# Kernel optimization log

Measured on AMD Instinct MI355X. Metric: run time of the kernel, lower is better.

## Reference

```python
import jax, jax.numpy as jnp
import numpy as np

B, C, H, W, D = 2, 256, 16, 16, 16
CQK = C // 8  # 32


def setup_inputs() -> dict:
    key = jax.random.key(0)
    ks = jax.random.split(key, 6)
    x = jax.random.normal(ks[0], (B, C, H, W, D), dtype=jnp.float32)
    wq = jax.random.normal(ks[1], (CQK, C), dtype=jnp.float32) * (1.0 / np.sqrt(C))
    wk = jax.random.normal(ks[2], (CQK, C), dtype=jnp.float32) * (1.0 / np.sqrt(C))
    wv = jax.random.normal(ks[3], (C, C), dtype=jnp.float32) * (1.0 / np.sqrt(C))
    bq = jnp.zeros((CQK,), dtype=jnp.float32)
    bk = jnp.zeros((CQK,), dtype=jnp.float32)
    bv = jnp.zeros((C,), dtype=jnp.float32)
    gamma_pam = jax.random.normal(ks[4], (1,), dtype=jnp.float32)
    gamma_cam = jax.random.normal(ks[5], (1,), dtype=jnp.float32)
    return {"x": x, "wq": wq, "bq": bq, "wk": wk, "bk": bk,
            "wv": wv, "bv": bv, "gamma_pam": gamma_pam, "gamma_cam": gamma_cam}


def _da_block(x, wq, bq, wk, bk, wv, bv, gamma_pam, gamma_cam):
    b, c, h, w, d = x.shape
    n = h * w * d
    xf = x.reshape(b, c, n)  # (B, C, N)

    # ---- PAM (position attention) ----
    # 1x1x1 Conv3d == per-voxel channel matmul
    q = jnp.einsum('oc,bcn->bon', wq, xf) + bq[None, :, None]  # (B, CQK, N)
    k = jnp.einsum('oc,bcn->bon', wk, xf) + bk[None, :, None]  # (B, CQK, N)
    v = jnp.einsum('oc,bcn->bon', wv, xf) + bv[None, :, None]  # (B, C, N)
    energy = jnp.einsum('bci,bcj->bij', q, k)                  # (B, N, N)
    attn = jax.nn.softmax(energy, axis=-1)
    # out[b,c,i] = sum_j v[b,c,j] * attn[b,i,j]
    pam_out = jnp.einsum('bcj,bij->bci', v, attn)              # (B, C, N)
    x1 = gamma_pam[0] * pam_out.reshape(b, c, h, w, d) + x

    # ---- CAM (channel attention, max-inverted energy) ----
    energy_c = jnp.einsum('bin,bjn->bij', xf, xf)              # (B, C, C)
    energy_new = jnp.max(energy_c, axis=-1, keepdims=True) - energy_c
    attn_c = jax.nn.softmax(energy_new, axis=-1)
    cam_out = jnp.einsum('bij,bjn->bin', attn_c, xf)           # (B, C, N)
    x2 = gamma_cam[0] * cam_out.reshape(b, c, h, w, d) + x

    return x1 + x2


def reference(x, wq, bq, wk, bk, wv, bv, gamma_pam, gamma_cam):
    return _da_block(x, wq, bq, wk, bk, wv, bv, gamma_pam, gamma_cam)
```

## Files before the change

### kernel.cpp

```cpp
#include <hip/hip_runtime.h>
#include <hip/hip_bf16.h>


#define B_ 2
#define C_ 256
#define N_ 4096
#define QK_ 32

#define TJ_ 128
#define PPB_ 136

typedef __hip_bfloat16 bf16;
typedef __attribute__((ext_vector_type(8))) short bf16x8f;
typedef __attribute__((ext_vector_type(4))) float f32x4;

union bf8pack { bf16 h[8]; int4 v; bf16x8f f; };
union bf4pack { bf16 h[4]; uint2 u; };

__global__ __launch_bounds__(256) void k_wcv(
    const float* __restrict__ wq, const float* __restrict__ wk, const float* __restrict__ wv,
    bf16* __restrict__ wqkh, bf16* __restrict__ wqkl,
    bf16* __restrict__ wvh, bf16* __restrict__ wvl) {
  int idx = blockIdx.x * 256 + threadIdx.x;
  if (idx < 64 * C_) {
    int r = idx >> 8, c = idx & 255;
    float v = (r < 32) ? wq[r * C_ + c] : wk[(r - 32) * C_ + c];
    bf16 h = __float2bfloat16(v);
    wqkh[idx] = h; wqkl[idx] = __float2bfloat16(v - __bfloat162float(h));
  } else {
    int j = idx - 64 * C_;
    float v = wv[j];
    bf16 h = __float2bfloat16(v);
    wvh[j] = h; wvl[j] = __float2bfloat16(v - __bfloat162float(h));
  }
}

__global__ __launch_bounds__(256) void k_xt(
    const float* __restrict__ x, bf16* __restrict__ xthi, bf16* __restrict__ xtlo,
    bf16* __restrict__ xchi, bf16* __restrict__ xclo) {
  int b = blockIdx.z;
  int c0 = blockIdx.y * 64;
  int n0 = blockIdx.x * 64;
  __shared__ float t[64 * 65];
  int tid = threadIdx.x;
  int col = tid & 63, rowq = tid >> 6;
#pragma unroll
  for (int k = 0; k < 16; k++) {
    int r = k * 4 + rowq;
    size_t src = ((size_t)b * C_ + c0 + r) * N_ + n0 + col;
    float v = x[src];
    t[r * 65 + col] = v;
    bf16 h = __float2bfloat16(v);
    xchi[src] = h;
    xclo[src] = __float2bfloat16(v - __bfloat162float(h));
  }
  __syncthreads();
#pragma unroll
  for (int k = 0; k < 16; k++) {
    int nrow = k * 4 + rowq;
    float v = t[col * 65 + nrow];
    bf16 h = __float2bfloat16(v);
    size_t o = ((size_t)b * N_ + n0 + nrow) * C_ + c0 + col;
    xthi[o] = h;
    xtlo[o] = __float2bfloat16(v - __bfloat162float(h));
  }
}

__global__ __launch_bounds__(256) void k_qkp(
    const bf16* __restrict__ xthi, const bf16* __restrict__ xtlo,
    const bf16* __restrict__ wqkh, const bf16* __restrict__ wqkl,
    const float* __restrict__ bq, const float* __restrict__ bk,
    bf16* __restrict__ qhi, bf16* __restrict__ qlo,
    bf16* __restrict__ khi, bf16* __restrict__ klo) {
  int b = blockIdx.y;
  int tid = threadIdx.x;
  int lane = tid & 63, wave = tid >> 6;
  int n16 = lane & 15, quad = lane >> 4;
  int nb = blockIdx.x * 128 + wave * 32;

  f32x4 acc[4][2];
#pragma unroll
  for (int ot = 0; ot < 4; ot++)
#pragma unroll
    for (int nt = 0; nt < 2; nt++) acc[ot][nt] = (f32x4)(0.f);

#pragma unroll
  for (int kk = 0; kk < 8; kk++) {
    bf16x8f Ah[4], Al[4], Bh[2], Bl[2];
#pragma unroll
    for (int ot = 0; ot < 4; ot++) {
      size_t off = (size_t)(ot * 16 + n16) * C_ + kk * 32 + quad * 8;
      Ah[ot] = *(const bf16x8f*)(const void*)(wqkh + off);
      Al[ot] = *(const bf16x8f*)(const void*)(wqkl + off);
    }
#pragma unroll
    for (int nt = 0; nt < 2; nt++) {
      size_t off = ((size_t)b * N_ + nb + nt * 16 + n16) * C_ + kk * 32 + quad * 8;
      Bh[nt] = *(const bf16x8f*)(const void*)(xthi + off);
      Bl[nt] = *(const bf16x8f*)(const void*)(xtlo + off);
    }
#pragma unroll
    for (int ot = 0; ot < 4; ot++)
#pragma unroll
      for (int nt = 0; nt < 2; nt++) {
        acc[ot][nt] = __builtin_amdgcn_mfma_f32_16x16x32_bf16(Ah[ot], Bh[nt], acc[ot][nt], 0, 0, 0);
        acc[ot][nt] = __builtin_amdgcn_mfma_f32_16x16x32_bf16(Al[ot], Bh[nt], acc[ot][nt], 0, 0, 0);
        acc[ot][nt] = __builtin_amdgcn_mfma_f32_16x16x32_bf16(Ah[ot], Bl[nt], acc[ot][nt], 0, 0, 0);
      }
  }
#pragma unroll
  for (int ot = 0; ot < 4; ot++)
#pragma unroll
    for (int nt = 0; nt < 2; nt++) {
      int n = nb + nt * 16 + n16;
      int o0 = (ot & 1) * 16 + quad * 4;
      bf4pack ph, pl;
#pragma unroll
      for (int r = 0; r < 4; r++) {
        float v = acc[ot][nt][r] + (ot < 2 ? bq[o0 + r] : bk[o0 + r]);
        bf16 h = __float2bfloat16(v);
        ph.h[r] = h; pl.h[r] = __float2bfloat16(v - __bfloat162float(h));
      }
      size_t base = ((size_t)b * N_ + n) * QK_ + o0;
      if (ot < 2) { *(uint2*)(qhi + base) = ph.u; *(uint2*)(qlo + base) = pl.u; }
      else        { *(uint2*)(khi + base) = ph.u; *(uint2*)(klo + base) = pl.u; }
    }
}

__global__ __launch_bounds__(256) void k_vbf2(
    const bf16* __restrict__ xthi, const bf16* __restrict__ xtlo,
    const bf16* __restrict__ wvh, const bf16* __restrict__ wvl,
    const float* __restrict__ bv, bf16* __restrict__ vbf) {
  int b = blockIdx.y;
  int n0 = blockIdx.x * 32;
  int tid = threadIdx.x;
  int lane = tid & 63, wave = tid >> 6;
  int n16 = lane & 15, quad = lane >> 4;
  int c0 = wave * 64;

  f32x4 acc[4][2];
#pragma unroll
  for (int ct = 0; ct < 4; ct++)
#pragma unroll
    for (int nt = 0; nt < 2; nt++) acc[ct][nt] = (f32x4)(0.f);

#pragma unroll
  for (int kk = 0; kk < 8; kk++) {
    bf16x8f Ah[4], Al[4], Bh[2], Bl[2];
#pragma unroll
    for (int ct = 0; ct < 4; ct++) {
      size_t off = (size_t)(c0 + ct * 16 + n16) * C_ + kk * 32 + quad * 8;
      Ah[ct] = *(const bf16x8f*)(const void*)(wvh + off);
      Al[ct] = *(const bf16x8f*)(const void*)(wvl + off);
    }
#pragma unroll
    for (int nt = 0; nt < 2; nt++) {
      size_t off = ((size_t)b * N_ + n0 + nt * 16 + n16) * C_ + kk * 32 + quad * 8;
      Bh[nt] = *(const bf16x8f*)(const void*)(xthi + off);
      Bl[nt] = *(const bf16x8f*)(const void*)(xtlo + off);
    }
#pragma unroll
    for (int ct = 0; ct < 4; ct++)
#pragma unroll
      for (int nt = 0; nt < 2; nt++) {
        acc[ct][nt] = __builtin_amdgcn_mfma_f32_16x16x32_bf16(Ah[ct], Bh[nt], acc[ct][nt], 0, 0, 0);
        acc[ct][nt] = __builtin_amdgcn_mfma_f32_16x16x32_bf16(Al[ct], Bh[nt], acc[ct][nt], 0, 0, 0);
        acc[ct][nt] = __builtin_amdgcn_mfma_f32_16x16x32_bf16(Ah[ct], Bl[nt], acc[ct][nt], 0, 0, 0);
      }
  }
#pragma unroll
  for (int ct = 0; ct < 4; ct++)
#pragma unroll
    for (int nt = 0; nt < 2; nt++) {
      int n = n0 + nt * 16 + n16;
      int cb = c0 + ct * 16 + quad * 4;
#pragma unroll
      for (int r = 0; r < 4; r++) {
        float v = acc[ct][nt][r] + bv[cb + r];
        vbf[((size_t)b * C_ + cb + r) * N_ + n] = __float2bfloat16(v);
      }
    }
}

__global__ __launch_bounds__(512) void k_pbm(
    const bf16* __restrict__ qhi, const bf16* __restrict__ qlo,
    const bf16* __restrict__ khi, const bf16* __restrict__ klo,
    const bf16* __restrict__ vbf,
    float* __restrict__ pamT) {
  int b = blockIdx.z;
  int h0 = blockIdx.y * 128;
  int i0 = blockIdx.x * 64;
  int tid = threadIdx.x;
  int lane = tid & 63, wave = tid >> 6;
  int n16 = lane & 15, quad = lane >> 4;

  __shared__ __align__(16) bf16 p_s[2][64 * PPB_];

  bf16x8f ahf[4], alf[4];
#pragma unroll
  for (int ih = 0; ih < 4; ih++) {
    size_t qoff = ((size_t)b * N_ + i0 + ih * 16 + n16) * QK_ + quad * 8;
    ahf[ih] = *(const bf16x8f*)(const void*)(qhi + qoff);
    alf[ih] = *(const bf16x8f*)(const void*)(qlo + qoff);
  }

  f32x4 acc[4];
  float l16[16];
#pragma unroll
  for (int ih = 0; ih < 4; ih++) acc[ih] = (f32x4)(0.f);
#pragma unroll
  for (int k = 0; k < 16; k++) l16[k] = 0.f;

  const bf16* khb = khi + ((size_t)b * N_ + wave * 16 + n16) * QK_ + quad * 8;
  const bf16* klb = klo + ((size_t)b * N_ + wave * 16 + n16) * QK_ + quad * 8;
  const bf16* vb0 = vbf + ((size_t)b * C_ + h0 + wave * 16 + n16) * N_ + quad * 8;

  const int NJT = N_ / TJ_;

  bf16x8f khf = *(const bf16x8f*)(const void*)khb;
  bf16x8f klf = *(const bf16x8f*)(const void*)klb;
  {
    bf16* pbuf = p_s[0];
#pragma unroll
    for (int ih = 0; ih < 4; ih++) {
      f32x4 t = (f32x4)(0.f);
      t = __builtin_amdgcn_mfma_f32_16x16x32_bf16(ahf[ih], khf, t, 0, 0, 0);
      t = __builtin_amdgcn_mfma_f32_16x16x32_bf16(alf[ih], khf, t, 0, 0, 0);
      t = __builtin_amdgcn_mfma_f32_16x16x32_bf16(ahf[ih], klf, t, 0, 0, 0);
#pragma unroll
      for (int r = 0; r < 4; r++) {
        int i = ih * 16 + quad * 4 + r;
        float p = __expf(t[r]);
        l16[ih * 4 + r] += p;
        pbuf[i * PPB_ + wave * 16 + n16] = __float2bfloat16(p);
      }
    }
  }
  khf = *(const bf16x8f*)(const void*)(khb + (size_t)TJ_ * QK_);
  klf = *(const bf16x8f*)(const void*)(klb + (size_t)TJ_ * QK_);
  bf16x8f vcur[4];
#pragma unroll
  for (int jhh = 0; jhh < 4; jhh++)
    vcur[jhh] = *(const bf16x8f*)(const void*)(vb0 + jhh * 32);
  __syncthreads();

  for (int jt = 0; jt < NJT; jt++) {
    f32x4 z[4];
    if (jt + 1 < NJT) {
#pragma unroll
      for (int ih = 0; ih < 4; ih++) {
        f32x4 t = (f32x4)(0.f);
        t = __builtin_amdgcn_mfma_f32_16x16x32_bf16(ahf[ih], khf, t, 0, 0, 0);
        t = __builtin_amdgcn_mfma_f32_16x16x32_bf16(alf[ih], khf, t, 0, 0, 0);
        t = __builtin_amdgcn_mfma_f32_16x16x32_bf16(ahf[ih], klf, t, 0, 0, 0);
        z[ih] = t;
      }
    }
    {
      const bf16* pbuf = p_s[jt & 1];
#pragma unroll
      for (int jhh = 0; jhh < 4; jhh++) {
        bf16x8f pa[4];
#pragma unroll
        for (int ih = 0; ih < 4; ih++)
          pa[ih] = *(const bf16x8f*)(const void*)(pbuf + (ih * 16 + n16) * PPB_ + jhh * 32 + quad * 8);
#pragma unroll
        for (int ih = 0; ih < 4; ih++)
          acc[ih] = __builtin_amdgcn_mfma_f32_16x16x32_bf16(pa[ih], vcur[jhh], acc[ih], 0, 0, 0);
      }
    }
    if (jt + 1 < NJT) {
      bf16* pbuf = p_s[(jt + 1) & 1];
#pragma unroll
      for (int ih = 0; ih < 4; ih++)
#pragma unroll
        for (int r = 0; r < 4; r++) {
          int i = ih * 16 + quad * 4 + r;
          float p = __expf(z[ih][r]);
          l16[ih * 4 + r] += p;
          pbuf[i * PPB_ + wave * 16 + n16] = __float2bfloat16(p);
        }
    }
    bf16x8f khn, kln, vnxt[4];
    if (jt + 2 < NJT) {
      size_t koff = (size_t)(jt + 2) * TJ_ * QK_;
      khn = *(const bf16x8f*)(const void*)(khb + koff);
      kln = *(const bf16x8f*)(const void*)(klb + koff);
    }
    if (jt + 1 < NJT) {
      int jb = (jt + 1) * TJ_;
#pragma unroll
      for (int jhh = 0; jhh < 4; jhh++)
        vnxt[jhh] = *(const bf16x8f*)(const void*)(vb0 + jb + jhh * 32);
    }
    __syncthreads();
    khf = khn; klf = kln;
#pragma unroll
    for (int jhh = 0; jhh < 4; jhh++) vcur[jhh] = vnxt[jhh];
  }

#pragma unroll
  for (int d = 1; d < 16; d <<= 1)
#pragma unroll
    for (int k = 0; k < 16; k++)
      l16[k] += __shfl_xor(l16[k], d, 64);
  float* red = (float*)p_s;
  float* linv = red + 8 * 64;
  if (n16 == 0) {
#pragma unroll
    for (int ih = 0; ih < 4; ih++)
#pragma unroll
      for (int r = 0; r < 4; r++)
        red[wave * 64 + ih * 16 + quad * 4 + r] = l16[ih * 4 + r];
  }
  __syncthreads();
  if (tid < 64) {
    float L = 0.f;
#pragma unroll
    for (int w = 0; w < 8; w++) L += red[w * 64 + tid];
    linv[tid] = 1.0f / L;
  }
  __syncthreads();
  int c = h0 + wave * 16 + n16;
#pragma unroll
  for (int ih = 0; ih < 4; ih++)
#pragma unroll
    for (int r = 0; r < 4; r++) {
      int i = ih * 16 + quad * 4 + r;
      pamT[((size_t)b * N_ + i0 + i) * C_ + c] = acc[ih][r] * linv[i];
    }
}

__global__ __launch_bounds__(256) void k_ce2(
    const bf16* __restrict__ xchi, const bf16* __restrict__ xclo,
    float* __restrict__ eCp) {
  int b = blockIdx.z;
  int kc = blockIdx.y;
  int i0 = blockIdx.x * 32;
  int tid = threadIdx.x;
  int lane = tid & 63, wave = tid >> 6;
  int n16 = lane & 15, quad = lane >> 4;
  int j0 = wave * 64;

  f32x4 acc[2][4];
#pragma unroll
  for (int it = 0; it < 2; it++)
#pragma unroll
    for (int jt = 0; jt < 4; jt++) acc[it][jt] = (f32x4)(0.f);

  size_t kb = (size_t)kc * 512;
#pragma unroll 2
  for (int kk = 0; kk < 16; kk++) {
    bf16x8f Ah[2], Al[2], Bh[4], Bl[4];
#pragma unroll
    for (int it = 0; it < 2; it++) {
      size_t off = ((size_t)b * C_ + i0 + it * 16 + n16) * N_ + kb + kk * 32 + quad * 8;
      Ah[it] = *(const bf16x8f*)(const void*)(xchi + off);
      Al[it] = *(const bf16x8f*)(const void*)(xclo + off);
    }
#pragma unroll
    for (int jt = 0; jt < 4; jt++) {
      size_t off = ((size_t)b * C_ + j0 + jt * 16 + n16) * N_ + kb + kk * 32 + quad * 8;
      Bh[jt] = *(const bf16x8f*)(const void*)(xchi + off);
      Bl[jt] = *(const bf16x8f*)(const void*)(xclo + off);
    }
#pragma unroll
    for (int it = 0; it < 2; it++)
#pragma unroll
      for (int jt = 0; jt < 4; jt++) {
        acc[it][jt] = __builtin_amdgcn_mfma_f32_16x16x32_bf16(Ah[it], Bh[jt], acc[it][jt], 0, 0, 0);
        acc[it][jt] = __builtin_amdgcn_mfma_f32_16x16x32_bf16(Al[it], Bh[jt], acc[it][jt], 0, 0, 0);
        acc[it][jt] = __builtin_amdgcn_mfma_f32_16x16x32_bf16(Ah[it], Bl[jt], acc[it][jt], 0, 0, 0);
      }
  }
  float* dst = eCp + ((size_t)kc * B_ + b) * C_ * C_;
#pragma unroll
  for (int it = 0; it < 2; it++)
#pragma unroll
    for (int jt = 0; jt < 4; jt++) {
      int i = i0 + it * 16 + quad * 4;
      int j = j0 + jt * 16 + n16;
#pragma unroll
      for (int r = 0; r < 4; r++)
        dst[(size_t)(i + r) * C_ + j] = acc[it][jt][r];
    }
}

__global__ __launch_bounds__(256) void k_cs(
    const float* __restrict__ eCp, bf16* __restrict__ ahi, bf16* __restrict__ alo) {
  int row = blockIdx.x;
  int b = row >> 8, i = row & 255;
  int j = threadIdx.x;
  float e = 0.f;
#pragma unroll
  for (int kc = 0; kc < 8; kc++) e += eCp[(((size_t)kc * B_ + b) * C_ + i) * C_ + j];
  float ne = -e;
  __shared__ float buf[256];
  buf[j] = ne;
  __syncthreads();
  for (int st = 128; st >= 1; st >>= 1) {
    if (j < st) buf[j] = fmaxf(buf[j], buf[j + st]);
    __syncthreads();
  }
  float m = buf[0];
  __syncthreads();
  float p = __expf(ne - m);
  buf[j] = p;
  __syncthreads();
  for (int st = 128; st >= 1; st >>= 1) {
    if (j < st) buf[j] += buf[j + st];
    __syncthreads();
  }
  float v = p / buf[0];
  bf16 h = __float2bfloat16(v);
  ahi[(size_t)row * C_ + j] = h;
  alo[(size_t)row * C_ + j] = __float2bfloat16(v - __bfloat162float(h));
}

__global__ __launch_bounds__(512) void k_cam(
    const bf16* __restrict__ xthi, const bf16* __restrict__ xtlo,
    const bf16* __restrict__ ahi, const bf16* __restrict__ alo,
    const float* __restrict__ pamT, const float* __restrict__ x,
    const float* __restrict__ gpam, const float* __restrict__ gcam,
    float* __restrict__ out) {
  int b = blockIdx.y;
  int n0 = blockIdx.x * 32;
  int tid = threadIdx.x;
  int lane = tid & 63, wave = tid >> 6;
  int n16 = lane & 15, quad = lane >> 4;
  int c0 = wave * 32;

  f32x4 acc[2][2];
#pragma unroll
  for (int nt = 0; nt < 2; nt++)
#pragma unroll
    for (int ct = 0; ct < 2; ct++) acc[nt][ct] = (f32x4)(0.f);

#pragma unroll
  for (int kk = 0; kk < 8; kk++) {
    bf16x8f Ah[2], Al[2], Bh[2], Bl[2];
#pragma unroll
    for (int nt = 0; nt < 2; nt++) {
      size_t off = ((size_t)b * N_ + n0 + nt * 16 + n16) * C_ + kk * 32 + quad * 8;
      Ah[nt] = *(const bf16x8f*)(const void*)(xthi + off);
      Al[nt] = *(const bf16x8f*)(const void*)(xtlo + off);
    }
#pragma unroll
    for (int ct = 0; ct < 2; ct++) {
      size_t off = ((size_t)b * C_ + c0 + ct * 16 + n16) * C_ + kk * 32 + quad * 8;
      Bh[ct] = *(const bf16x8f*)(const void*)(ahi + off);
      Bl[ct] = *(const bf16x8f*)(const void*)(alo + off);
    }
#pragma unroll
    for (int nt = 0; nt < 2; nt++)
#pragma unroll
      for (int ct = 0; ct < 2; ct++) {
        acc[nt][ct] = __builtin_amdgcn_mfma_f32_16x16x32_bf16(Ah[nt], Bh[ct], acc[nt][ct], 0, 0, 0);
        acc[nt][ct] = __builtin_amdgcn_mfma_f32_16x16x32_bf16(Al[nt], Bh[ct], acc[nt][ct], 0, 0, 0);
        acc[nt][ct] = __builtin_amdgcn_mfma_f32_16x16x32_bf16(Ah[nt], Bl[ct], acc[nt][ct], 0, 0, 0);
      }
  }
  float gp = gpam[0], gc = gcam[0];
#pragma unroll
  for (int nt = 0; nt < 2; nt++)
#pragma unroll
    for (int ct = 0; ct < 2; ct++) {
      int c = c0 + ct * 16 + n16;
      int nb = n0 + nt * 16 + quad * 4;
      const float* xp = x + ((size_t)b * C_ + c) * N_ + nb;
      float4 x4 = *(const float4*)(const void*)xp;
      float4 o4;
      o4.x = gp * pamT[((size_t)b * N_ + nb + 0) * C_ + c] + gc * acc[nt][ct][0] + 2.0f * x4.x;
      o4.y = gp * pamT[((size_t)b * N_ + nb + 1) * C_ + c] + gc * acc[nt][ct][1] + 2.0f * x4.y;
      o4.z = gp * pamT[((size_t)b * N_ + nb + 2) * C_ + c] + gc * acc[nt][ct][2] + 2.0f * x4.z;
      o4.w = gp * pamT[((size_t)b * N_ + nb + 3) * C_ + c] + gc * acc[nt][ct][3] + 2.0f * x4.w;
      *(float4*)(out + ((size_t)b * C_ + c) * N_ + nb) = o4;
    }
}

extern "C" void kernel_launch(void* const* d_in, const int* in_sizes, int n_in,
                              void* d_out, int out_size, void* d_ws, size_t ws_size,
                              hipStream_t stream) {
  const float* x  = (const float*)d_in[0];
  const float* wq = (const float*)d_in[1];
  const float* bq = (const float*)d_in[2];
  const float* wk = (const float*)d_in[3];
  const float* bk = (const float*)d_in[4];
  const float* wv = (const float*)d_in[5];
  const float* bv = (const float*)d_in[6];
  const float* gp = (const float*)d_in[7];
  const float* gc = (const float*)d_in[8];
  float* out = (float*)d_out;

  float* ws = (float*)d_ws;
  size_t o = 0;
  float* pamT  = ws + o; o += (size_t)B_ * N_ * C_;
  float* mp    = ws + o; o += (size_t)2 * B_ * N_;
  float* lp    = ws + o; o += (size_t)2 * B_ * N_;
  float* eCp   = ws + o; o += (size_t)8 * B_ * C_ * C_;
  bf16*  ahi   = (bf16*)(ws + o); o += (size_t)B_ * C_ * C_ / 2;
  bf16*  alo   = (bf16*)(ws + o); o += (size_t)B_ * C_ * C_ / 2;
  bf16*  vbf   = (bf16*)(ws + o); o += (size_t)B_ * N_ * C_ / 2;
  bf16*  qhi   = (bf16*)(ws + o); o += (size_t)B_ * N_ * QK_ / 2;
  bf16*  qlo   = (bf16*)(ws + o); o += (size_t)B_ * N_ * QK_ / 2;
  bf16*  khi   = (bf16*)(ws + o); o += (size_t)B_ * N_ * QK_ / 2;
  bf16*  klo   = (bf16*)(ws + o); o += (size_t)B_ * N_ * QK_ / 2;
  float* xtbuf = ws + o; o += (size_t)2 * B_ * N_ * QK_ * 4;
  bf16* xthi = (bf16*)xtbuf;
  bf16* xtlo = (bf16*)(xtbuf + (size_t)B_ * N_ * C_ / 2);
  bf16* wqkh = (bf16*)eCp;
  bf16* wqkl = wqkh + (size_t)64 * C_;
  bf16* wvh  = wqkl + (size_t)64 * C_;
  bf16* wvl  = wvh + (size_t)C_ * C_;
  bf16* xchi = (bf16*)pamT;
  bf16* xclo = xchi + (size_t)B_ * C_ * N_;
  (void)mp; (void)lp;

  k_wcv<<<dim3((64 * C_ + C_ * C_) / 256), dim3(256), 0, stream>>>(wq, wk, wv, wqkh, wqkl, wvh, wvl);
  k_xt<<<dim3(N_ / 64, C_ / 64, B_), dim3(256), 0, stream>>>(x, xthi, xtlo, xchi, xclo);
  k_qkp<<<dim3(N_ / 128, B_), dim3(256), 0, stream>>>(xthi, xtlo, wqkh, wqkl, bq, bk, qhi, qlo, khi, klo);
  k_vbf2<<<dim3(N_ / 32, B_), dim3(256), 0, stream>>>(xthi, xtlo, wvh, wvl, bv, vbf);
  k_ce2<<<dim3(C_ / 32, 8, B_), dim3(256), 0, stream>>>(xchi, xclo, eCp);
  k_cs<<<dim3(B_ * C_), dim3(256), 0, stream>>>(eCp, ahi, alo);
  k_pbm<<<dim3(N_ / 64, 2, B_), dim3(512), 0, stream>>>(qhi, qlo, khi, klo, vbf, pamT);
  k_cam<<<dim3(N_ / 32, B_), dim3(512), 0, stream>>>(xthi, xtlo, ahi, alo, pamT, x, gp, gc, out);
}
```

Measured before the change: 202.6 us.

## Retile PAM kernel to cover all channels per block and swizzle P in LDS

The PAM attention kernel now gives each block 32 query rows and all 256 channels, instead of 64 rows and half the channels split across a grid y-dimension. The QK^T energy and exp work is no longer duplicated across the two channel halves, and each wave handles two 16-channel V blocks per P fragment. The P tile in shared memory uses an XOR-like rotation of its 8-element column blocks, intended to reduce LDS bank conflicts on the transposed reads. Each thread now holds more V registers, which may lower occupancy.

```diff
diff --git a/kernel.cpp b/kernel.cpp
--- a/kernel.cpp
+++ b/kernel.cpp
@@ -187,42 +187,45 @@
     const bf16* __restrict__ khi, const bf16* __restrict__ klo,
     const bf16* __restrict__ vbf,
     float* __restrict__ pamT) {
-  int b = blockIdx.z;
-  int h0 = blockIdx.y * 128;
-  int i0 = blockIdx.x * 64;
+  int b = blockIdx.y;
+  int i0 = blockIdx.x * 32;
   int tid = threadIdx.x;
   int lane = tid & 63, wave = tid >> 6;
   int n16 = lane & 15, quad = lane >> 4;
 
-  __shared__ __align__(16) bf16 p_s[2][64 * PPB_];
-
-  bf16x8f ahf[4], alf[4];
-#pragma unroll
-  for (int ih = 0; ih < 4; ih++) {
+  __shared__ __align__(16) bf16 p_s[2][32 * PPB_];
+
+  bf16x8f ahf[2], alf[2];
+#pragma unroll
+  for (int ih = 0; ih < 2; ih++) {
     size_t qoff = ((size_t)b * N_ + i0 + ih * 16 + n16) * QK_ + quad * 8;
     ahf[ih] = *(const bf16x8f*)(const void*)(qhi + qoff);
     alf[ih] = *(const bf16x8f*)(const void*)(qlo + qoff);
   }
 
-  f32x4 acc[4];
-  float l16[16];
-#pragma unroll
-  for (int ih = 0; ih < 4; ih++) acc[ih] = (f32x4)(0.f);
-#pragma unroll
-  for (int k = 0; k < 16; k++) l16[k] = 0.f;
+  f32x4 acc[2][2];
+  float l8[8];
+#pragma unroll
+  for (int ih = 0; ih < 2; ih++)
+#pragma unroll
+    for (int cb = 0; cb < 2; cb++) acc[ih][cb] = (f32x4)(0.f);
+#pragma unroll
+  for (int k = 0; k < 8; k++) l8[k] = 0.f;
 
   const bf16* khb = khi + ((size_t)b * N_ + wave * 16 + n16) * QK_ + quad * 8;
   const bf16* klb = klo + ((size_t)b * N_ + wave * 16 + n16) * QK_ + quad * 8;
-  const bf16* vb0 = vbf + ((size_t)b * C_ + h0 + wave * 16 + n16) * N_ + quad * 8;
+  const bf16* vb0 = vbf + ((size_t)b * C_ + wave * 32 + n16) * N_ + quad * 8;
 
   const int NJT = N_ / TJ_;
+  int wcol = wave * 16 + n16;
+  int wblk = wcol >> 3, wrem = wcol & 7;
 
   bf16x8f khf = *(const bf16x8f*)(const void*)khb;
   bf16x8f klf = *(const bf16x8f*)(const void*)klb;
   {
     bf16* pbuf = p_s[0];
 #pragma unroll
-    for (int ih = 0; ih < 4; ih++) {
+    for (int ih = 0; ih < 2; ih++) {
       f32x4 t = (f32x4)(0.f);
       t = __builtin_amdgcn_mfma_f32_16x16x32_bf16(ahf[ih], khf, t, 0, 0, 0);
       t = __builtin_amdgcn_mfma_f32_16x16x32_bf16(alf[ih], khf, t, 0, 0, 0);
@@ -231,24 +234,26 @@
       for (int r = 0; r < 4; r++) {
         int i = ih * 16 + quad * 4 + r;
         float p = __expf(t[r]);
-        l16[ih * 4 + r] += p;
-        pbuf[i * PPB_ + wave * 16 + n16] = __float2bfloat16(p);
+        l8[ih * 4 + r] += p;
+        pbuf[i * PPB_ + (((wblk + i) & 15) << 3) + wrem] = __float2bfloat16(p);
       }
     }
   }
   khf = *(const bf16x8f*)(const void*)(khb + (size_t)TJ_ * QK_);
   klf = *(const bf16x8f*)(const void*)(klb + (size_t)TJ_ * QK_);
-  bf16x8f vcur[4];
-#pragma unroll
-  for (int jhh = 0; jhh < 4; jhh++)
-    vcur[jhh] = *(const bf16x8f*)(const void*)(vb0 + jhh * 32);
+  bf16x8f vcur[2][4];
+#pragma unroll
+  for (int cb = 0; cb < 2; cb++)
+#pragma unroll
+    for (int jhh = 0; jhh < 4; jhh++)
+      vcur[cb][jhh] = *(const bf16x8f*)(const void*)(vb0 + (size_t)cb * 16 * N_ + jhh * 32);
   __syncthreads();
 
   for (int jt = 0; jt < NJT; jt++) {
-    f32x4 z[4];
+    f32x4 z[2];
     if (jt + 1 < NJT) {
 #pragma unroll
-      for (int ih = 0; ih < 4; ih++) {
+      for (int ih = 0; ih < 2; ih++) {
         f32x4 t = (f32x4)(0.f);
         t = __builtin_amdgcn_mfma_f32_16x16x32_bf16(ahf[ih], khf, t, 0, 0, 0);
         t = __builtin_amdgcn_mfma_f32_16x16x32_bf16(alf[ih], khf, t, 0, 0, 0);
@@ -260,28 +265,33 @@
       const bf16* pbuf = p_s[jt & 1];
 #pragma unroll
       for (int jhh = 0; jhh < 4; jhh++) {
-        bf16x8f pa[4];
-#pragma unroll
-        for (int ih = 0; ih < 4; ih++)
-          pa[ih] = *(const bf16x8f*)(const void*)(pbuf + (ih * 16 + n16) * PPB_ + jhh * 32 + quad * 8);
-#pragma unroll
-        for (int ih = 0; ih < 4; ih++)
-          acc[ih] = __builtin_amdgcn_mfma_f32_16x16x32_bf16(pa[ih], vcur[jhh], acc[ih], 0, 0, 0);
+        int jb = jhh * 4 + quad;
+        bf16x8f pa[2];
+#pragma unroll
+        for (int ih = 0; ih < 2; ih++) {
+          int ir = ih * 16 + n16;
+          pa[ih] = *(const bf16x8f*)(const void*)(pbuf + ir * PPB_ + (((jb + ir) & 15) << 3));
+        }
+#pragma unroll
+        for (int ih = 0; ih < 2; ih++)
+#pragma unroll
+          for (int cb = 0; cb < 2; cb++)
+            acc[ih][cb] = __builtin_amdgcn_mfma_f32_16x16x32_bf16(pa[ih], vcur[cb][jhh], acc[ih][cb], 0, 0, 0);
       }
     }
     if (jt + 1 < NJT) {
       bf16* pbuf = p_s[(jt + 1) & 1];
 #pragma unroll
-      for (int ih = 0; ih < 4; ih++)
+      for (int ih = 0; ih < 2; ih++)
 #pragma unroll
         for (int r = 0; r < 4; r++) {
           int i = ih * 16 + quad * 4 + r;
           float p = __expf(z[ih][r]);
-          l16[ih * 4 + r] += p;
-          pbuf[i * PPB_ + wave * 16 + n16] = __float2bfloat16(p);
+          l8[ih * 4 + r] += p;
+          pbuf[i * PPB_ + (((wblk + i) & 15) << 3) + wrem] = __float2bfloat16(p);
         }
     }
-    bf16x8f khn, kln, vnxt[4];
+    bf16x8f khn, kln, vnxt[2][4];
     if (jt + 2 < NJT) {
       size_t koff = (size_t)(jt + 2) * TJ_ * QK_;
       khn = *(const bf16x8f*)(const void*)(khb + koff);
@@ -290,44 +300,51 @@
     if (jt + 1 < NJT) {
       int jb = (jt + 1) * TJ_;
 #pragma unroll
-      for (int jhh = 0; jhh < 4; jhh++)
-        vnxt[jhh] = *(const bf16x8f*)(const void*)(vb0 + jb + jhh * 32);
+      for (int cb = 0; cb < 2; cb++)
+#pragma unroll
+        for (int jhh = 0; jhh < 4; jhh++)
+          vnxt[cb][jhh] = *(const bf16x8f*)(const void*)(vb0 + (size_t)cb * 16 * N_ + jb + jhh * 32);
     }
     __syncthreads();
     khf = khn; klf = kln;
 #pragma unroll
-    for (int jhh = 0; jhh < 4; jhh++) vcur[jhh] = vnxt[jhh];
+    for (int cb = 0; cb < 2; cb++)
+#pragma unroll
+      for (int jhh = 0; jhh < 4; jhh++) vcur[cb][jhh] = vnxt[cb][jhh];
   }
 
 #pragma unroll
   for (int d = 1; d < 16; d <<= 1)
 #pragma unroll
-    for (int k = 0; k < 16; k++)
-      l16[k] += __shfl_xor(l16[k], d, 64);
+    for (int k = 0; k < 8; k++)
+      l8[k] += __shfl_xor(l8[k], d, 64);
   float* red = (float*)p_s;
-  float* linv = red + 8 * 64;
+  float* linv = red + 8 * 32;
   if (n16 == 0) {
 #pragma unroll
-    for (int ih = 0; ih < 4; ih++)
+    for (int ih = 0; ih < 2; ih++)
 #pragma unroll
       for (int r = 0; r < 4; r++)
-        red[wave * 64 + ih * 16 + quad * 4 + r] = l16[ih * 4 + r];
-  }
-  __syncthreads();
-  if (tid < 64) {
+        red[wave * 32 + ih * 16 + quad * 4 + r] = l8[ih * 4 + r];
+  }
+  __syncthreads();
+  if (tid < 32) {
     float L = 0.f;
 #pragma unroll
-    for (int w = 0; w < 8; w++) L += red[w * 64 + tid];
+    for (int w = 0; w < 8; w++) L += red[w * 32 + tid];
     linv[tid] = 1.0f / L;
   }
   __syncthreads();
-  int c = h0 + wave * 16 + n16;
-#pragma unroll
-  for (int ih = 0; ih < 4; ih++)
-#pragma unroll
-    for (int r = 0; r < 4; r++) {
-      int i = ih * 16 + quad * 4 + r;
-      pamT[((size_t)b * N_ + i0 + i) * C_ + c] = acc[ih][r] * linv[i];
+#pragma unroll
+  for (int ih = 0; ih < 2; ih++)
+#pragma unroll
+    for (int cb = 0; cb < 2; cb++) {
+      int c = wave * 32 + cb * 16 + n16;
+#pragma unroll
+      for (int r = 0; r < 4; r++) {
+        int i = ih * 16 + quad * 4 + r;
+        pamT[((size_t)b * N_ + i0 + i) * C_ + c] = acc[ih][cb][r] * linv[i];
+      }
     }
 }
 
@@ -522,6 +539,6 @@
   k_vbf2<<<dim3(N_ / 32, B_), dim3(256), 0, stream>>>(xthi, xtlo, wvh, wvl, bv, vbf);
   k_ce2<<<dim3(C_ / 32, 8, B_), dim3(256), 0, stream>>>(xchi, xclo, eCp);
   k_cs<<<dim3(B_ * C_), dim3(256), 0, stream>>>(eCp, ahi, alo);
-  k_pbm<<<dim3(N_ / 64, 2, B_), dim3(512), 0, stream>>>(qhi, qlo, khi, klo, vbf, pamT);
+  k_pbm<<<dim3(N_ / 32, B_), dim3(512), 0, stream>>>(qhi, qlo, khi, klo, vbf, pamT);
   k_cam<<<dim3(N_ / 32, B_), dim3(512), 0, stream>>>(xthi, xtlo, ahi, alo, pamT, x, gp, gc, out);
 }
```

Result: slower. 224.6 us (+10.9%).

## Split PAM over key halves with atomic accumulation and swizzled P tile

Applied to the files above, without the earlier changes.

The PAM kernel now splits the key/value range into two halves across blockIdx.y instead of splitting output channels. Each block covers all 256 channels, so the exp(QK) scores are computed once per key instead of twice. Partial outputs and row sums are combined with float atomics into pamT and lsum, which k_cs zeroes beforehand, and the softmax normalisation moves into k_cam. The shared P buffer layout is XOR-style swizzled to reduce LDS bank conflicts. The cost is atomic traffic on pamT, and the summation order becomes nondeterministic.

```diff
diff --git a/kernel.cpp b/kernel.cpp
--- a/kernel.cpp
+++ b/kernel.cpp
@@ -186,9 +186,10 @@
     const bf16* __restrict__ qhi, const bf16* __restrict__ qlo,
     const bf16* __restrict__ khi, const bf16* __restrict__ klo,
     const bf16* __restrict__ vbf,
-    float* __restrict__ pamT) {
+    float* __restrict__ pamT, float* __restrict__ lsum) {
   int b = blockIdx.z;
-  int h0 = blockIdx.y * 128;
+  int jh = blockIdx.y;
+  size_t j0 = (size_t)jh * (N_ / 2);
   int i0 = blockIdx.x * 64;
   int tid = threadIdx.x;
   int lane = tid & 63, wave = tid >> 6;
@@ -204,18 +205,22 @@
     alf[ih] = *(const bf16x8f*)(const void*)(qlo + qoff);
   }
 
-  f32x4 acc[4];
+  f32x4 acc[4][2];
   float l16[16];
 #pragma unroll
-  for (int ih = 0; ih < 4; ih++) acc[ih] = (f32x4)(0.f);
+  for (int ih = 0; ih < 4; ih++)
+#pragma unroll
+    for (int cb = 0; cb < 2; cb++) acc[ih][cb] = (f32x4)(0.f);
 #pragma unroll
   for (int k = 0; k < 16; k++) l16[k] = 0.f;
 
-  const bf16* khb = khi + ((size_t)b * N_ + wave * 16 + n16) * QK_ + quad * 8;
-  const bf16* klb = klo + ((size_t)b * N_ + wave * 16 + n16) * QK_ + quad * 8;
-  const bf16* vb0 = vbf + ((size_t)b * C_ + h0 + wave * 16 + n16) * N_ + quad * 8;
-
-  const int NJT = N_ / TJ_;
+  const bf16* khb = khi + ((size_t)b * N_ + j0 + wave * 16 + n16) * QK_ + quad * 8;
+  const bf16* klb = klo + ((size_t)b * N_ + j0 + wave * 16 + n16) * QK_ + quad * 8;
+  const bf16* vb0 = vbf + ((size_t)b * C_ + wave * 32 + n16) * N_ + j0 + quad * 8;
+
+  const int NJT = (N_ / 2) / TJ_;
+  int wcol = wave * 16 + n16;
+  int wblk = wcol >> 3, wrem = wcol & 7;
 
   bf16x8f khf = *(const bf16x8f*)(const void*)khb;
   bf16x8f klf = *(const bf16x8f*)(const void*)klb;
@@ -232,16 +237,18 @@
         int i = ih * 16 + quad * 4 + r;
         float p = __expf(t[r]);
         l16[ih * 4 + r] += p;
-        pbuf[i * PPB_ + wave * 16 + n16] = __float2bfloat16(p);
+        pbuf[i * PPB_ + (((wblk + i) & 15) << 3) + wrem] = __float2bfloat16(p);
       }
     }
   }
   khf = *(const bf16x8f*)(const void*)(khb + (size_t)TJ_ * QK_);
   klf = *(const bf16x8f*)(const void*)(klb + (size_t)TJ_ * QK_);
-  bf16x8f vcur[4];
-#pragma unroll
-  for (int jhh = 0; jhh < 4; jhh++)
-    vcur[jhh] = *(const bf16x8f*)(const void*)(vb0 + jhh * 32);
+  bf16x8f vcur[2][4];
+#pragma unroll
+  for (int cb = 0; cb < 2; cb++)
+#pragma unroll
+    for (int jhh = 0; jhh < 4; jhh++)
+      vcur[cb][jhh] = *(const bf16x8f*)(const void*)(vb0 + (size_t)cb * 16 * N_ + jhh * 32);
   __syncthreads();
 
   for (int jt = 0; jt < NJT; jt++) {
@@ -260,13 +267,18 @@
       const bf16* pbuf = p_s[jt & 1];
 #pragma unroll
       for (int jhh = 0; jhh < 4; jhh++) {
+        int jb = jhh * 4 + quad;
         bf16x8f pa[4];
 #pragma unroll
+        for (int ih = 0; ih < 4; ih++) {
+          int ir = ih * 16 + n16;
+          pa[ih] = *(const bf16x8f*)(const void*)(pbuf + ir * PPB_ + (((jb + ir) & 15) << 3));
+        }
+#pragma unroll
         for (int ih = 0; ih < 4; ih++)
-          pa[ih] = *(const bf16x8f*)(const void*)(pbuf + (ih * 16 + n16) * PPB_ + jhh * 32 + quad * 8);
-#pragma unroll
-        for (int ih = 0; ih < 4; ih++)
-          acc[ih] = __builtin_amdgcn_mfma_f32_16x16x32_bf16(pa[ih], vcur[jhh], acc[ih], 0, 0, 0);
+#pragma unroll
+          for (int cb = 0; cb < 2; cb++)
+            acc[ih][cb] = __builtin_amdgcn_mfma_f32_16x16x32_bf16(pa[ih], vcur[cb][jhh], acc[ih][cb], 0, 0, 0);
       }
     }
     if (jt + 1 < NJT) {
@@ -278,10 +290,10 @@
           int i = ih * 16 + quad * 4 + r;
           float p = __expf(z[ih][r]);
           l16[ih * 4 + r] += p;
-          pbuf[i * PPB_ + wave * 16 + n16] = __float2bfloat16(p);
+          pbuf[i * PPB_ + (((wblk + i) & 15) << 3) + wrem] = __float2bfloat16(p);
         }
     }
-    bf16x8f khn, kln, vnxt[4];
+    bf16x8f khn, kln, vnxt[2][4];
     if (jt + 2 < NJT) {
       size_t koff = (size_t)(jt + 2) * TJ_ * QK_;
       khn = *(const bf16x8f*)(const void*)(khb + koff);
@@ -290,13 +302,17 @@
     if (jt + 1 < NJT) {
       int jb = (jt + 1) * TJ_;
 #pragma unroll
-      for (int jhh = 0; jhh < 4; jhh++)
-        vnxt[jhh] = *(const bf16x8f*)(const void*)(vb0 + jb + jhh * 32);
+      for (int cb = 0; cb < 2; cb++)
+#pragma unroll
+        for (int jhh = 0; jhh < 4; jhh++)
+          vnxt[cb][jhh] = *(const bf16x8f*)(const void*)(vb0 + (size_t)cb * 16 * N_ + jb + jhh * 32);
     }
     __syncthreads();
     khf = khn; klf = kln;
 #pragma unroll
-    for (int jhh = 0; jhh < 4; jhh++) vcur[jhh] = vnxt[jhh];
+    for (int cb = 0; cb < 2; cb++)
+#pragma unroll
+      for (int jhh = 0; jhh < 4; jhh++) vcur[cb][jhh] = vnxt[cb][jhh];
   }
 
 #pragma unroll
@@ -305,7 +321,6 @@
     for (int k = 0; k < 16; k++)
       l16[k] += __shfl_xor(l16[k], d, 64);
   float* red = (float*)p_s;
-  float* linv = red + 8 * 64;
   if (n16 == 0) {
 #pragma unroll
     for (int ih = 0; ih < 4; ih++)
@@ -318,16 +333,18 @@
     float L = 0.f;
 #pragma unroll
     for (int w = 0; w < 8; w++) L += red[w * 64 + tid];
-    linv[tid] = 1.0f / L;
-  }
-  __syncthreads();
-  int c = h0 + wave * 16 + n16;
+    unsafeAtomicAdd(&lsum[(size_t)b * N_ + i0 + tid], L);
+  }
 #pragma unroll
   for (int ih = 0; ih < 4; ih++)
 #pragma unroll
-    for (int r = 0; r < 4; r++) {
-      int i = ih * 16 + quad * 4 + r;
-      pamT[((size_t)b * N_ + i0 + i) * C_ + c] = acc[ih][r] * linv[i];
+    for (int cb = 0; cb < 2; cb++) {
+      int c = wave * 32 + cb * 16 + n16;
+#pragma unroll
+      for (int r = 0; r < 4; r++) {
+        int i = ih * 16 + quad * 4 + r;
+        unsafeAtomicAdd(&pamT[((size_t)b * N_ + i0 + i) * C_ + c], acc[ih][cb][r]);
+      }
     }
 }
 
@@ -387,10 +404,18 @@
 }
 
 __global__ __launch_bounds__(256) void k_cs(
-    const float* __restrict__ eCp, bf16* __restrict__ ahi, bf16* __restrict__ alo) {
+    const float* __restrict__ eCp, bf16* __restrict__ ahi, bf16* __restrict__ alo,
+    float* __restrict__ pamZ, float* __restrict__ lsum) {
   int row = blockIdx.x;
   int b = row >> 8, i = row & 255;
   int j = threadIdx.x;
+  {
+    int t = row * 256 + j;
+    float4* pz = (float4*)(pamZ + (size_t)t * 16);
+    float4 z4 = make_float4(0.f, 0.f, 0.f, 0.f);
+    pz[0] = z4; pz[1] = z4; pz[2] = z4; pz[3] = z4;
+    if (t < B_ * N_) lsum[t] = 0.f;
+  }
   float e = 0.f;
 #pragma unroll
   for (int kc = 0; kc < 8; kc++) e += eCp[(((size_t)kc * B_ + b) * C_ + i) * C_ + j];
@@ -420,7 +445,8 @@
 __global__ __launch_bounds__(512) void k_cam(
     const bf16* __restrict__ xthi, const bf16* __restrict__ xtlo,
     const bf16* __restrict__ ahi, const bf16* __restrict__ alo,
-    const float* __restrict__ pamT, const float* __restrict__ x,
+    const float* __restrict__ pamT, const float* __restrict__ lsum,
+    const float* __restrict__ x,
     const float* __restrict__ gpam, const float* __restrict__ gcam,
     float* __restrict__ out) {
   int b = blockIdx.y;
@@ -461,6 +487,14 @@
       }
   }
   float gp = gpam[0], gc = gcam[0];
+  float linv[2][4];
+#pragma unroll
+  for (int nt = 0; nt < 2; nt++) {
+    int nb = n0 + nt * 16 + quad * 4;
+#pragma unroll
+    for (int r = 0; r < 4; r++)
+      linv[nt][r] = 1.0f / lsum[(size_t)b * N_ + nb + r];
+  }
 #pragma unroll
   for (int nt = 0; nt < 2; nt++)
 #pragma unroll
@@ -470,10 +504,10 @@
       const float* xp = x + ((size_t)b * C_ + c) * N_ + nb;
       float4 x4 = *(const float4*)(const void*)xp;
       float4 o4;
-      o4.x = gp * pamT[((size_t)b * N_ + nb + 0) * C_ + c] + gc * acc[nt][ct][0] + 2.0f * x4.x;
-      o4.y = gp * pamT[((size_t)b * N_ + nb + 1) * C_ + c] + gc * acc[nt][ct][1] + 2.0f * x4.y;
-      o4.z = gp * pamT[((size_t)b * N_ + nb + 2) * C_ + c] + gc * acc[nt][ct][2] + 2.0f * x4.z;
-      o4.w = gp * pamT[((size_t)b * N_ + nb + 3) * C_ + c] + gc * acc[nt][ct][3] + 2.0f * x4.w;
+      o4.x = gp * pamT[((size_t)b * N_ + nb + 0) * C_ + c] * linv[nt][0] + gc * acc[nt][ct][0] + 2.0f * x4.x;
+      o4.y = gp * pamT[((size_t)b * N_ + nb + 1) * C_ + c] * linv[nt][1] + gc * acc[nt][ct][1] + 2.0f * x4.y;
+      o4.z = gp * pamT[((size_t)b * N_ + nb + 2) * C_ + c] * linv[nt][2] + gc * acc[nt][ct][2] + 2.0f * x4.z;
+      o4.w = gp * pamT[((size_t)b * N_ + nb + 3) * C_ + c] * linv[nt][3] + gc * acc[nt][ct][3] + 2.0f * x4.w;
       *(float4*)(out + ((size_t)b * C_ + c) * N_ + nb) = o4;
     }
 }
@@ -495,7 +529,7 @@
   float* ws = (float*)d_ws;
   size_t o = 0;
   float* pamT  = ws + o; o += (size_t)B_ * N_ * C_;
-  float* mp    = ws + o; o += (size_t)2 * B_ * N_;
+  float* lsum  = ws + o; o += (size_t)2 * B_ * N_;
   float* lp    = ws + o; o += (size_t)2 * B_ * N_;
   float* eCp   = ws + o; o += (size_t)8 * B_ * C_ * C_;
   bf16*  ahi   = (bf16*)(ws + o); o += (size_t)B_ * C_ * C_ / 2;
@@ -514,14 +548,14 @@
   bf16* wvl  = wvh + (size_t)C_ * C_;
   bf16* xchi = (bf16*)pamT;
   bf16* xclo = xchi + (size_t)B_ * C_ * N_;
-  (void)mp; (void)lp;
+  (void)lp;
 
   k_wcv<<<dim3((64 * C_ + C_ * C_) / 256), dim3(256), 0, stream>>>(wq, wk, wv, wqkh, wqkl, wvh, wvl);
   k_xt<<<dim3(N_ / 64, C_ / 64, B_), dim3(256), 0, stream>>>(x, xthi, xtlo, xchi, xclo);
   k_qkp<<<dim3(N_ / 128, B_), dim3(256), 0, stream>>>(xthi, xtlo, wqkh, wqkl, bq, bk, qhi, qlo, khi, klo);
   k_vbf2<<<dim3(N_ / 32, B_), dim3(256), 0, stream>>>(xthi, xtlo, wvh, wvl, bv, vbf);
   k_ce2<<<dim3(C_ / 32, 8, B_), dim3(256), 0, stream>>>(xchi, xclo, eCp);
-  k_cs<<<dim3(B_ * C_), dim3(256), 0, stream>>>(eCp, ahi, alo);
-  k_pbm<<<dim3(N_ / 64, 2, B_), dim3(512), 0, stream>>>(qhi, qlo, khi, klo, vbf, pamT);
-  k_cam<<<dim3(N_ / 32, B_), dim3(512), 0, stream>>>(xthi, xtlo, ahi, alo, pamT, x, gp, gc, out);
-}
+  k_cs<<<dim3(B_ * C_), dim3(256), 0, stream>>>(eCp, ahi, alo, pamT, lsum);
+  k_pbm<<<dim3(N_ / 64, 2, B_), dim3(512), 0, stream>>>(qhi, qlo, khi, klo, vbf, pamT, lsum);
+  k_cam<<<dim3(N_ / 32, B_), dim3(512), 0, stream>>>(xthi, xtlo, ahi, alo, pamT, lsum, x, gp, gc, out);
+}
```

New measurement: 211.3 us. 4.3% more time.
